# Optimization experiments

Measured on AMD Instinct MI355X. Metric: run time of the kernel, lower is better.

Reference implementation:

```python
import jax, jax.numpy as jnp
import numpy as np

DIM = 192
HEADS = 4


def setup_inputs() -> dict:
    key = jax.random.key(0)
    ks = jax.random.split(key, 6)
    b, h, w = 8, 128, 128
    return {
        "x": jax.random.normal(ks[0], (b, DIM, h, w), jnp.float32),
        "svp_fea": jax.random.normal(ks[1], (b, 3, h, w), jnp.float32),
        "qkv_w": jax.random.normal(ks[2], (3 * DIM, DIM), jnp.float32) * 0.02,
        "dw_w": jax.random.normal(ks[3], (3 * DIM, 1, 3, 3), jnp.float32) * 0.02,
        "svp_w": jax.random.normal(ks[4], (3 * HEADS, 3), jnp.float32) * 0.02,
        "proj_w": jax.random.normal(ks[5], (DIM, DIM + 3 * HEADS), jnp.float32) * 0.02,
        "temperature": jnp.ones((HEADS, 1, 1), jnp.float32),
    }


def _l2norm(t):
    # F.normalize(t, dim=-1): divide by max(||t||_2, eps)
    return t / jnp.maximum(jnp.linalg.norm(t, axis=-1, keepdims=True), 1e-12)


def reference(x, svp_fea, qkv_w, dw_w, svp_w, proj_w, temperature):
    b, c, h, w = x.shape
    heads = temperature.shape[0]
    # 1x1 conv (dim -> 3*dim), then 3x3 depthwise conv (groups = 3*dim)
    qkv = jnp.einsum('bchw,oc->bohw', x, qkv_w)
    qkv = jax.lax.conv_general_dilated(
        qkv, dw_w, window_strides=(1, 1), padding=((1, 1), (1, 1)),
        dimension_numbers=('NCHW', 'OIHW', 'NCHW'), feature_group_count=3 * c)
    # 1x1 conv on illumination prior: 3 -> 3*heads
    svp_q = jnp.einsum('bchw,oc->bohw', svp_fea, svp_w)
    q, k, v = jnp.split(qkv, 3, axis=1)
    ch = c // heads
    hw = h * w
    q = _l2norm(q.reshape(b, heads, ch, hw))
    k = _l2norm(k.reshape(b, heads, ch, hw))
    v = v.reshape(b, heads, ch, hw)
    sq = _l2norm(svp_q.reshape(b, heads, 3, hw))
    q = jnp.concatenate([q, sq], axis=2)            # [b, head, ch+3, hw]
    logits = jnp.einsum('bhcn,bhdn->bhcd', q, k) * temperature[None]
    attn = jax.nn.softmax(logits, axis=-1)          # softmax over channel dim d
    out = jnp.einsum('bhcd,bhdn->bhcn', attn, v)    # [b, head, ch+3, hw]
    out = out.reshape(b, heads * (ch + 3), h, w)
    return jnp.einsum('bchw,oc->bohw', out, proj_w)
```

## Files before the change

kernel.cpp:

```cpp
#include <hip/hip_runtime.h>
#include <hip/hip_bf16.h>
#include <math.h>

#define BB   8
#define CCH  192
#define OCN  576
#define HWD  128
#define HWN  16384
#define NH   4
#define CHD  48
#define C51  51
#define GSZ  (C51*48)

typedef __hip_bfloat16 bf16;
typedef __attribute__((ext_vector_type(8))) short short8;
typedef __attribute__((ext_vector_type(4))) float f32x4;

__device__ __forceinline__ float bfbits2f(unsigned int u16) {
  union { unsigned int i; float f; } v; v.i = u16 << 16; return v.f;
}
__device__ __forceinline__ unsigned short f2bfbits(float f) {
  __hip_bfloat16 h = __float2bfloat16(f);
  return *(unsigned short*)&h;
}
__device__ __forceinline__ void stage16(const void* g, void* l) {
  __builtin_amdgcn_global_load_lds(
      (const __attribute__((address_space(1))) void*)g,
      (__attribute__((address_space(3))) void*)l, 16, 0, 0);
}

__global__ __launch_bounds__(256) void k_svp(
    const float* __restrict__ svp_fea, const float* __restrict__ svp_w,
    float* __restrict__ svp_q, float* __restrict__ ssq_svp_p)
{
  __shared__ float lsw[4][12];
  const int b = blockIdx.y;
  const int t = threadIdx.x;
  const int n = blockIdx.x * 256 + t;
  const int wave = t >> 6;
  const float* fb = svp_fea + (size_t)b * 3 * HWN;
  const float f0 = fb[n], f1 = fb[HWN + n], f2 = fb[2 * HWN + n];
  float* ob = svp_q + (size_t)b * 12 * HWN + n;
  #pragma unroll
  for (int r = 0; r < 12; ++r) {
    float o = svp_w[r*3]*f0 + svp_w[r*3+1]*f1 + svp_w[r*3+2]*f2;
    ob[(size_t)r * HWN] = o;
    float v = o * o;
    #pragma unroll
    for (int off = 32; off >= 1; off >>= 1) v += __shfl_down(v, off, 64);
    if ((t & 63) == 0) lsw[wave][r] = v;
  }
  __syncthreads();
  if (t < 12) {
    float s = lsw[0][t] + lsw[1][t] + lsw[2][t] + lsw[3][t];
    ssq_svp_p[((size_t)b * 12 + t) * 64 + blockIdx.x] = s;
  }
}

__global__ __launch_bounds__(256) void k_castw(
    const float* __restrict__ w, unsigned short* __restrict__ wb)
{
  const int i = (blockIdx.x * 256 + threadIdx.x) * 4;
  float4 v = *(const float4*)(w + i);
  union { uint2 u; unsigned short s[4]; } pk;
  pk.s[0] = f2bfbits(v.x); pk.s[1] = f2bfbits(v.y);
  pk.s[2] = f2bfbits(v.z); pk.s[3] = f2bfbits(v.w);
  *(uint2*)(wb + i) = pk.u;
}

__global__ __launch_bounds__(256) void k_gemm(
    const float* __restrict__ x, const unsigned short* __restrict__ wb,
    unsigned short* __restrict__ qkv1)
{
  __shared__ unsigned short Xs[64 * CCH];
  __shared__ unsigned short Wd[2][32 * CCH];
  const int b = blockIdx.y;
  const int n0 = blockIdx.x * 64;
  const int t = threadIdx.x;
  const int lane = t & 63, wave = t >> 6;
  const int wm = wave >> 1, wn = wave & 1;
  const int lq = lane >> 4, lr = lane & 15;

  #pragma unroll
  for (int i = 0; i < 3; ++i) {
    int chunk = wave * 3 + i;
    int d = chunk * 64 + lane;
    int row = d / 24, kg = d % 24;
    int skg = (kg & ~7) | ((kg & 7) ^ (row & 7));
    stage16(wb + (size_t)row * CCH + skg * 8, &Wd[0][0] + chunk * 512);
  }

  const float* xb = x + (size_t)b * CCH * HWN + n0;
  #pragma unroll
  for (int rr = 0; rr < 6; ++rr) {
    int idx = rr * 256 + t;
    int cp = idx >> 4, nq = idx & 15;
    int c0 = cp * 2;
    float4 v0 = *(const float4*)(xb + (size_t)c0 * HWN + nq * 4);
    float4 v1 = *(const float4*)(xb + (size_t)(c0 + 1) * HWN + nq * 4);
    int g = c0 >> 3, co = c0 & 7;
    float a0[4] = {v0.x, v0.y, v0.z, v0.w};
    float a1[4] = {v1.x, v1.y, v1.z, v1.w};
    #pragma unroll
    for (int j = 0; j < 4; ++j) {
      int n = nq * 4 + j;
      int gs = (g & ~7) | ((g & 7) ^ (n & 7) ^ ((n >> 3) & 7));
      unsigned int pk = (unsigned int)f2bfbits(a0[j])
                      | ((unsigned int)f2bfbits(a1[j]) << 16);
      *(unsigned int*)&Xs[n * CCH + gs * 8 + co] = pk;
    }
  }
  __syncthreads();

  short8 bfr[2][6];
  #pragma unroll
  for (int nf = 0; nf < 2; ++nf) {
    int r = wn * 32 + nf * 16 + lr;
    #pragma unroll
    for (int ks = 0; ks < 6; ++ks) {
      int gk = ks * 4 + lq;
      int sg = (gk & ~7) | ((gk & 7) ^ (r & 7) ^ ((r >> 3) & 7));
      bfr[nf][ks] = *(const short8*)&Xs[r * CCH + sg * 8];
    }
  }

  for (int mc = 0; mc < 18; ++mc) {
    if (mc + 1 < 18) {
      const unsigned short* wsrc = wb + (size_t)(mc + 1) * 32 * CCH;
      unsigned short* nb = &Wd[(mc + 1) & 1][0];
      #pragma unroll
      for (int i = 0; i < 3; ++i) {
        int chunk = wave * 3 + i;
        int d = chunk * 64 + lane;
        int row = d / 24, kg = d % 24;
        int skg = (kg & ~7) | ((kg & 7) ^ (row & 7));
        stage16(wsrc + (size_t)row * CCH + skg * 8, nb + chunk * 512);
      }
      asm volatile("s_waitcnt vmcnt(3)" ::: "memory");
    } else {
      asm volatile("s_waitcnt vmcnt(0)" ::: "memory");
    }
    __builtin_amdgcn_s_barrier();
    asm volatile("" ::: "memory");

    const unsigned short* wbuf = &Wd[mc & 1][0];
    f32x4 acc0 = (f32x4)0.f, acc1 = (f32x4)0.f;
    #pragma unroll
    for (int ks = 0; ks < 6; ++ks) {
      const int gk = ks * 4 + lq;
      int r = wm * 16 + lr;
      int sg = (gk & ~7) | ((gk & 7) ^ (r & 7));
      short8 a = *(const short8*)&wbuf[r * CCH + sg * 8];
      acc0 = __builtin_amdgcn_mfma_f32_16x16x32_bf16(a, bfr[0][ks], acc0, 0, 0, 0);
      acc1 = __builtin_amdgcn_mfma_f32_16x16x32_bf16(a, bfr[1][ks], acc1, 0, 0, 0);
    }

    unsigned short* ob = qkv1 + ((size_t)b * OCN + mc * 32 + wm * 16) * HWN
                         + n0 + wn * 32;
    #pragma unroll
    for (int r = 0; r < 4; ++r) {
      ob[(size_t)(lq * 4 + r) * HWN + lr]      = f2bfbits(acc0[r]);
      ob[(size_t)(lq * 4 + r) * HWN + 16 + lr] = f2bfbits(acc1[r]);
    }
    asm volatile("" ::: "memory");
    __builtin_amdgcn_s_barrier();
  }
}

__global__ __launch_bounds__(256) void k_dw(
    const unsigned short* __restrict__ qkv1, const float* __restrict__ dw_w,
    unsigned short* __restrict__ qkv, float* __restrict__ ssq_qk_p)
{
  __shared__ float lsw[4];
  const int b = blockIdx.z, c = blockIdx.y, slab = blockIdx.x;
  const int t = threadIdx.x;
  const int cg = t & 15, rg = t >> 4;
  const int y0 = slab * 32 + rg * 2;
  const unsigned short* src = qkv1 + ((size_t)b * OCN + c) * HWN;
  float w[9];
  #pragma unroll
  for (int i = 0; i < 9; ++i) w[i] = dw_w[c * 9 + i];

  float rows[4][10];
  #pragma unroll
  for (int j = 0; j < 4; ++j) {
    int gr = y0 - 1 + j;
    uint4 B = make_uint4(0u, 0u, 0u, 0u);
    unsigned int Al = 0; unsigned int Cv = 0;
    if ((unsigned)gr < 128u) {
      const unsigned short* rp = src + (size_t)gr * HWD;
      B = *(const uint4*)(rp + cg * 8);
      if (cg > 0)  Al = *(const unsigned int*)(rp + cg * 8 - 2);
      if (cg < 15) Cv = (unsigned int)rp[cg * 8 + 8];
    }
    rows[j][0] = bfbits2f(Al >> 16);
    unsigned int ub[4] = {B.x, B.y, B.z, B.w};
    #pragma unroll
    for (int q = 0; q < 4; ++q) {
      rows[j][1 + 2*q] = bfbits2f(ub[q] & 0xffffu);
      rows[j][2 + 2*q] = bfbits2f(ub[q] >> 16);
    }
    rows[j][9] = bfbits2f(Cv);
  }

  unsigned short* dst = qkv + ((size_t)b * OCN + c) * HWN;
  float ssq = 0.f;
  #pragma unroll
  for (int e = 0; e < 2; ++e) {
    float acc[8];
    #pragma unroll
    for (int i = 0; i < 8; ++i) acc[i] = 0.f;
    #pragma unroll
    for (int j = 0; j < 3; ++j) {
      const float* vr = rows[e + j];
      #pragma unroll
      for (int i = 0; i < 8; ++i)
        acc[i] += w[j*3]*vr[i] + w[j*3+1]*vr[i+1] + w[j*3+2]*vr[i+2];
    }
    union { uint4 u; unsigned short s[8]; } pk;
    #pragma unroll
    for (int i = 0; i < 8; ++i) pk.s[i] = f2bfbits(acc[i]);
    *(uint4*)(dst + (size_t)(y0 + e) * HWD + cg * 8) = pk.u;
    if (c < 384) {
      #pragma unroll
      for (int i = 0; i < 8; ++i) {
        float rv = bfbits2f(pk.s[i]);
        ssq += rv * rv;
      }
    }
  }
  if (c < 384) {
    #pragma unroll
    for (int off = 32; off >= 1; off >>= 1) ssq += __shfl_down(ssq, off, 64);
    if ((t & 63) == 0) lsw[t >> 6] = ssq;
  }
  __syncthreads();
  if (c < 384 && t == 0)
    ssq_qk_p[(((size_t)b * 384 + c) << 2) | slab] =
        lsw[0] + lsw[1] + lsw[2] + lsw[3];
}

__global__ __launch_bounds__(256) void k_gram(
    const unsigned short* __restrict__ qkv, const float* __restrict__ svp_q,
    float* __restrict__ Gp)
{
  __shared__ float Gs[C51 * 50];
  const int chunk = blockIdx.x, h = blockIdx.y, b = blockIdx.z;
  const int t = threadIdx.x;
  const int lane = t & 63, wave = t >> 6;
  const int lq = lane >> 4, lr = lane & 15;
  const unsigned short* qb = qkv + ((size_t)b*OCN + h*CHD)*HWN;
  const unsigned short* kb = qkv + ((size_t)b*OCN + 192 + h*CHD)*HWN;
  const float* sb = svp_q + ((size_t)b*12 + h*3)*HWN;

  for (int idx = t; idx < C51*50; idx += 256) Gs[idx] = 0.f;

  f32x4 acc[3][3], sacc[3];
  #pragma unroll
  for (int mf = 0; mf < 3; ++mf)
    #pragma unroll
    for (int nf = 0; nf < 3; ++nf) acc[mf][nf] = (f32x4)0.f;
  #pragma unroll
  for (int nf = 0; nf < 3; ++nf) sacc[nf] = (f32x4)0.f;

  const int nbase = chunk * 1024 + wave * 256;
  #pragma unroll 4
  for (int ks = 0; ks < 8; ++ks) {
    const int n = nbase + ks * 32 + lq * 8;
    short8 a[3], bb[3];
    #pragma unroll
    for (int mf = 0; mf < 3; ++mf)
      a[mf] = *(const short8*)&qb[(size_t)(mf*16 + lr)*HWN + n];
    #pragma unroll
    for (int nf = 0; nf < 3; ++nf)
      bb[nf] = *(const short8*)&kb[(size_t)(nf*16 + lr)*HWN + n];
    union { short8 s8; unsigned short us[8]; } sv;
    #pragma unroll
    for (int i = 0; i < 8; ++i) sv.us[i] = 0;
    if (lr < 3) {
      const float* sp = sb + (size_t)lr*HWN + n;
      float4 v0 = *(const float4*)sp, v1 = *(const float4*)(sp + 4);
      sv.us[0] = f2bfbits(v0.x); sv.us[1] = f2bfbits(v0.y);
      sv.us[2] = f2bfbits(v0.z); sv.us[3] = f2bfbits(v0.w);
      sv.us[4] = f2bfbits(v1.x); sv.us[5] = f2bfbits(v1.y);
      sv.us[6] = f2bfbits(v1.z); sv.us[7] = f2bfbits(v1.w);
    }
    #pragma unroll
    for (int mf = 0; mf < 3; ++mf)
      #pragma unroll
      for (int nf = 0; nf < 3; ++nf)
        acc[mf][nf] = __builtin_amdgcn_mfma_f32_16x16x32_bf16(
            a[mf], bb[nf], acc[mf][nf], 0, 0, 0);
    #pragma unroll
    for (int nf = 0; nf < 3; ++nf)
      sacc[nf] = __builtin_amdgcn_mfma_f32_16x16x32_bf16(
          sv.s8, bb[nf], sacc[nf], 0, 0, 0);
  }

  __syncthreads();
  for (int w = 0; w < 4; ++w) {
    if (wave == w) {
      #pragma unroll
      for (int mf = 0; mf < 3; ++mf)
        #pragma unroll
        for (int nf = 0; nf < 3; ++nf)
          #pragma unroll
          for (int r = 0; r < 4; ++r)
            Gs[(mf*16 + lq*4 + r)*50 + nf*16 + lr] += acc[mf][nf][r];
      if (lq == 0) {
        #pragma unroll
        for (int nf = 0; nf < 3; ++nf)
          #pragma unroll
          for (int r = 0; r < 3; ++r)
            Gs[(48 + r)*50 + nf*16 + lr] += sacc[nf][r];
      }
    }
    __syncthreads();
  }
  float* Gout = Gp + ((size_t)((b*NH + h) * 16 + chunk)) * GSZ;
  for (int idx = t; idx < GSZ; idx += 256) {
    int row = idx / 48, col = idx - row * 48;
    Gout[idx] = Gs[row*50 + col];
  }
}

__global__ __launch_bounds__(256) void k_attn_fold(
    const float* __restrict__ Gp, const float* __restrict__ ssq_qk_p,
    const float* __restrict__ ssq_svp_p, const float* __restrict__ temperature,
    const float* __restrict__ proj_w, unsigned short* __restrict__ W2bf)
{
  __shared__ float A[GSZ];
  __shared__ float qinv[C51];
  __shared__ float kinv[48];
  const int h = blockIdx.x, b = blockIdx.y;
  const int t = threadIdx.x;
  const float* Gb = Gp + ((size_t)(b*NH + h) * 16) * GSZ;
  if (t < 48) {
    const float* p = ssq_qk_p + (((size_t)b * 384 + 192 + h*48 + t) << 2);
    kinv[t] = 1.f / fmaxf(sqrtf(p[0] + p[1] + p[2] + p[3]), 1e-12f);
  }
  if (t >= 64 && t < 64 + C51) {
    int c = t - 64;
    float ss;
    if (c < 48) {
      const float* p = ssq_qk_p + (((size_t)b * 384 + h*48 + c) << 2);
      ss = p[0] + p[1] + p[2] + p[3];
    } else {
      const float* p = ssq_svp_p + ((size_t)b * 12 + h*3 + (c - 48)) * 64;
      float s0 = 0.f, s1 = 0.f, s2 = 0.f, s3 = 0.f;
      #pragma unroll
      for (int i = 0; i < 16; ++i) {
        float4 v = *(const float4*)(p + i * 4);
        s0 += v.x; s1 += v.y; s2 += v.z; s3 += v.w;
      }
      ss = (s0 + s1) + (s2 + s3);
    }
    qinv[c] = 1.f / fmaxf(sqrtf(ss), 1e-12f);
  }
  for (int idx = t; idx < GSZ; idx += 256) {
    float s = 0.f;
    #pragma unroll
    for (int c = 0; c < 16; ++c) s += Gb[(size_t)c * GSZ + idx];
    A[idx] = s;
  }
  __syncthreads();
  const float temp = temperature[h];
  if (t < C51) {
    float row[48];
    float m = -1e30f;
    const float qi = qinv[t] * temp;
    #pragma unroll
    for (int d = 0; d < 48; ++d) {
      float l = A[t*48 + d] * qi * kinv[d];
      row[d] = l; m = fmaxf(m, l);
    }
    float s = 0.f;
    #pragma unroll
    for (int d = 0; d < 48; ++d) { row[d] = expf(row[d] - m); s += row[d]; }
    const float inv = 1.f / s;
    #pragma unroll
    for (int d = 0; d < 48; ++d) A[t*48 + d] = row[d] * inv;
  }
  __syncthreads();
  for (int idx = t; idx < 192*48; idx += 256) {
    int o = idx / 48, d = idx - o*48;
    const float* pw = proj_w + o*204 + C51*h;
    float s = 0.f;
    #pragma unroll
    for (int c = 0; c < C51; ++c) s += pw[c] * A[c*48 + d];
    W2bf[((size_t)b*CCH + o)*CCH + h*48 + d] = f2bfbits(s);
  }
}

__global__ __launch_bounds__(256) void k_out(
    const unsigned short* __restrict__ qkv, const unsigned short* __restrict__ w2b,
    float* __restrict__ out)
{
  __shared__ unsigned short Vs[64 * CCH];
  __shared__ unsigned short Wd[2][32 * CCH];
  const int b = blockIdx.y;
  const int n0 = blockIdx.x * 64;
  const int t = threadIdx.x;
  const int lane = t & 63, wave = t >> 6;
  const int wm = wave >> 1, wn = wave & 1;
  const int lq = lane >> 4, lr = lane & 15;

  const unsigned short* w2base = w2b + (size_t)b * CCH * CCH;
  #pragma unroll
  for (int i = 0; i < 3; ++i) {
    int chunk = wave * 3 + i;
    int d = chunk * 64 + lane;
    int row = d / 24, kg = d % 24;
    int skg = (kg & ~7) | ((kg & 7) ^ (row & 7));
    stage16(w2base + (size_t)row * CCH + skg * 8, &Wd[0][0] + chunk * 512);
  }

  const unsigned short* vb = qkv + ((size_t)b * OCN + 384) * HWN + n0;
  #pragma unroll
  for (int rr = 0; rr < 3; ++rr) {
    int idx = rr * 256 + t;
    int cp = idx >> 3, nq = idx & 7;
    int c0 = cp * 2;
    uint4 v0 = *(const uint4*)(vb + (size_t)c0 * HWN + nq * 8);
    uint4 v1 = *(const uint4*)(vb + (size_t)(c0 + 1) * HWN + nq * 8);
    union { uint4 u; unsigned short s[8]; } p0, p1;
    p0.u = v0; p1.u = v1;
    int g = c0 >> 3, co = c0 & 7;
    #pragma unroll
    for (int j = 0; j < 8; ++j) {
      int n = nq * 8 + j;
      int gs = (g & ~7) | ((g & 7) ^ (n & 7) ^ ((n >> 3) & 7));
      unsigned int pk = (unsigned int)p0.s[j] | ((unsigned int)p1.s[j] << 16);
      *(unsigned int*)&Vs[n * CCH + gs * 8 + co] = pk;
    }
  }
  __syncthreads();

  short8 bfr[2][6];
  #pragma unroll
  for (int nf = 0; nf < 2; ++nf) {
    int r = wn * 32 + nf * 16 + lr;
    #pragma unroll
    for (int ks = 0; ks < 6; ++ks) {
      int gk = ks * 4 + lq;
      int sg = (gk & ~7) | ((gk & 7) ^ (r & 7) ^ ((r >> 3) & 7));
      bfr[nf][ks] = *(const short8*)&Vs[r * CCH + sg * 8];
    }
  }

  for (int mc = 0; mc < 6; ++mc) {
    if (mc + 1 < 6) {
      const unsigned short* wsrc = w2base + (size_t)(mc + 1) * 32 * CCH;
      unsigned short* nb = &Wd[(mc + 1) & 1][0];
      #pragma unroll
      for (int i = 0; i < 3; ++i) {
        int chunk = wave * 3 + i;
        int d = chunk * 64 + lane;
        int row = d / 24, kg = d % 24;
        int skg = (kg & ~7) | ((kg & 7) ^ (row & 7));
        stage16(wsrc + (size_t)row * CCH + skg * 8, nb + chunk * 512);
      }
      asm volatile("s_waitcnt vmcnt(3)" ::: "memory");
    } else {
      asm volatile("s_waitcnt vmcnt(0)" ::: "memory");
    }
    __builtin_amdgcn_s_barrier();
    asm volatile("" ::: "memory");

    const unsigned short* wbuf = &Wd[mc & 1][0];
    f32x4 acc0 = (f32x4)0.f, acc1 = (f32x4)0.f;
    #pragma unroll
    for (int ks = 0; ks < 6; ++ks) {
      const int gk = ks * 4 + lq;
      int r = wm * 16 + lr;
      int sg = (gk & ~7) | ((gk & 7) ^ (r & 7));
      short8 a = *(const short8*)&wbuf[r * CCH + sg * 8];
      acc0 = __builtin_amdgcn_mfma_f32_16x16x32_bf16(a, bfr[0][ks], acc0, 0, 0, 0);
      acc1 = __builtin_amdgcn_mfma_f32_16x16x32_bf16(a, bfr[1][ks], acc1, 0, 0, 0);
    }

    float* ob = out + ((size_t)b * CCH + mc * 32 + wm * 16) * HWN + n0 + wn * 32;
    #pragma unroll
    for (int r = 0; r < 4; ++r) {
      ob[(size_t)(lq * 4 + r) * HWN + lr]      = acc0[r];
      ob[(size_t)(lq * 4 + r) * HWN + 16 + lr] = acc1[r];
    }
    asm volatile("" ::: "memory");
    __builtin_amdgcn_s_barrier();
  }
}

extern "C" void kernel_launch(void* const* d_in, const int* in_sizes, int n_in,
                              void* d_out, int out_size, void* d_ws, size_t ws_size,
                              hipStream_t stream)
{
  const float* x       = (const float*)d_in[0];
  const float* svp_fea = (const float*)d_in[1];
  const float* qkv_w   = (const float*)d_in[2];
  const float* dw_w    = (const float*)d_in[3];
  const float* svp_w   = (const float*)d_in[4];
  const float* proj_w  = (const float*)d_in[5];
  const float* temp    = (const float*)d_in[6];
  float* outp = (float*)d_out;

  char* ws = (char*)d_ws;
  const size_t off_qkv1   = 0;
  const size_t off_qkv    = off_qkv1  + (size_t)BB*OCN*HWN*2;
  const size_t off_wb     = off_qkv   + (size_t)BB*OCN*HWN*2;
  const size_t off_svpq   = off_wb    + (size_t)OCN*CCH*2;
  const size_t off_ssqqk  = off_svpq  + (size_t)BB*12*HWN*4;
  const size_t off_ssqsvp = off_ssqqk + (size_t)BB*384*4*4;
  const size_t off_Gp     = off_ssqsvp+ (size_t)BB*12*64*4;
  const size_t off_W2     = off_Gp    + (size_t)BB*NH*16*GSZ*4;

  unsigned short* qkv1  = (unsigned short*)(ws + off_qkv1);
  bf16*  qkv     = (bf16*)(ws + off_qkv);
  unsigned short* wb    = (unsigned short*)(ws + off_wb);
  float* svp_q   = (float*)(ws + off_svpq);
  float* ssq_qk_p  = (float*)(ws + off_ssqqk);
  float* ssq_svp_p = (float*)(ws + off_ssqsvp);
  float* Gp      = (float*)(ws + off_Gp);
  unsigned short* W2bf  = (unsigned short*)(ws + off_W2);

  k_castw    <<<dim3(108),         256, 0, stream>>>(qkv_w, wb);
  k_svp      <<<dim3(64, BB),      256, 0, stream>>>(svp_fea, svp_w, svp_q, ssq_svp_p);
  k_gemm     <<<dim3(256, BB),     256, 0, stream>>>(x, wb, qkv1);
  k_dw       <<<dim3(4, OCN, BB),  256, 0, stream>>>(qkv1, dw_w, (unsigned short*)qkv, ssq_qk_p);
  k_gram     <<<dim3(16, NH, BB),  256, 0, stream>>>((const unsigned short*)qkv, svp_q, Gp);
  k_attn_fold<<<dim3(NH, BB),      256, 0, stream>>>(Gp, ssq_qk_p, ssq_svp_p, temp, proj_w, W2bf);
  k_out      <<<dim3(256, BB),     256, 0, stream>>>((const unsigned short*)qkv, W2bf, outp);
}
```

Baseline: 279.5 us.

## Widen QKV GEMM pixel tile and swap MFMA operands for vectorized stores

```diff
diff --git a/kernel.cpp b/kernel.cpp
--- a/kernel.cpp
+++ b/kernel.cpp
@@ -72,10 +72,10 @@
     const float* __restrict__ x, const unsigned short* __restrict__ wb,
     unsigned short* __restrict__ qkv1)
 {
-  __shared__ unsigned short Xs[64 * CCH];
+  __shared__ unsigned short Xs[128 * CCH];
   __shared__ unsigned short Wd[2][32 * CCH];
   const int b = blockIdx.y;
-  const int n0 = blockIdx.x * 64;
+  const int n0 = blockIdx.x * 128;
   const int t = threadIdx.x;
   const int lane = t & 63, wave = t >> 6;
   const int wm = wave >> 1, wn = wave & 1;
@@ -92,9 +92,9 @@
 
   const float* xb = x + (size_t)b * CCH * HWN + n0;
   #pragma unroll
-  for (int rr = 0; rr < 6; ++rr) {
+  for (int rr = 0; rr < 12; ++rr) {
     int idx = rr * 256 + t;
-    int cp = idx >> 4, nq = idx & 15;
+    int cp = idx >> 5, nq = idx & 31;
     int c0 = cp * 2;
     float4 v0 = *(const float4*)(xb + (size_t)c0 * HWN + nq * 4);
     float4 v1 = *(const float4*)(xb + (size_t)(c0 + 1) * HWN + nq * 4);
@@ -112,10 +112,10 @@
   }
   __syncthreads();
 
-  short8 bfr[2][6];
-  #pragma unroll
-  for (int nf = 0; nf < 2; ++nf) {
-    int r = wn * 32 + nf * 16 + lr;
+  short8 bfr[4][6];
+  #pragma unroll
+  for (int nf = 0; nf < 4; ++nf) {
+    int r = wn * 64 + nf * 16 + lr;
     #pragma unroll
     for (int ks = 0; ks < 6; ++ks) {
       int gk = ks * 4 + lq;
@@ -144,23 +144,30 @@
     asm volatile("" ::: "memory");
 
     const unsigned short* wbuf = &Wd[mc & 1][0];
-    f32x4 acc0 = (f32x4)0.f, acc1 = (f32x4)0.f;
+    f32x4 acc[4];
+    #pragma unroll
+    for (int nf = 0; nf < 4; ++nf) acc[nf] = (f32x4)0.f;
+
     #pragma unroll
     for (int ks = 0; ks < 6; ++ks) {
       const int gk = ks * 4 + lq;
-      int r = wm * 16 + lr;
-      int sg = (gk & ~7) | ((gk & 7) ^ (r & 7));
-      short8 a = *(const short8*)&wbuf[r * CCH + sg * 8];
-      acc0 = __builtin_amdgcn_mfma_f32_16x16x32_bf16(a, bfr[0][ks], acc0, 0, 0, 0);
-      acc1 = __builtin_amdgcn_mfma_f32_16x16x32_bf16(a, bfr[1][ks], acc1, 0, 0, 0);
-    }
-
-    unsigned short* ob = qkv1 + ((size_t)b * OCN + mc * 32 + wm * 16) * HWN
-                         + n0 + wn * 32;
-    #pragma unroll
-    for (int r = 0; r < 4; ++r) {
-      ob[(size_t)(lq * 4 + r) * HWN + lr]      = f2bfbits(acc0[r]);
-      ob[(size_t)(lq * 4 + r) * HWN + 16 + lr] = f2bfbits(acc1[r]);
+      int rW = wm * 16 + lr;
+      int sg = (gk & ~7) | ((gk & 7) ^ (rW & 7));
+      short8 w8 = *(const short8*)&wbuf[rW * CCH + sg * 8];
+      #pragma unroll
+      for (int nf = 0; nf < 4; ++nf)
+        acc[nf] = __builtin_amdgcn_mfma_f32_16x16x32_bf16(
+            bfr[nf][ks], w8, acc[nf], 0, 0, 0);
+    }
+
+    unsigned short* ob = qkv1 + ((size_t)b * OCN + mc * 32 + wm * 16 + lr) * HWN
+                         + n0 + wn * 64 + lq * 4;
+    #pragma unroll
+    for (int nf = 0; nf < 4; ++nf) {
+      union { uint2 u; unsigned short s[4]; } pk;
+      #pragma unroll
+      for (int r = 0; r < 4; ++r) pk.s[r] = f2bfbits(acc[nf][r]);
+      *(uint2*)(ob + nf * 16) = pk.u;
     }
     asm volatile("" ::: "memory");
     __builtin_amdgcn_s_barrier();
@@ -472,19 +479,17 @@
     #pragma unroll
     for (int ks = 0; ks < 6; ++ks) {
       const int gk = ks * 4 + lq;
-      int r = wm * 16 + lr;
-      int sg = (gk & ~7) | ((gk & 7) ^ (r & 7));
-      short8 a = *(const short8*)&wbuf[r * CCH + sg * 8];
-      acc0 = __builtin_amdgcn_mfma_f32_16x16x32_bf16(a, bfr[0][ks], acc0, 0, 0, 0);
-      acc1 = __builtin_amdgcn_mfma_f32_16x16x32_bf16(a, bfr[1][ks], acc1, 0, 0, 0);
-    }
-
-    float* ob = out + ((size_t)b * CCH + mc * 32 + wm * 16) * HWN + n0 + wn * 32;
-    #pragma unroll
-    for (int r = 0; r < 4; ++r) {
-      ob[(size_t)(lq * 4 + r) * HWN + lr]      = acc0[r];
-      ob[(size_t)(lq * 4 + r) * HWN + 16 + lr] = acc1[r];
-    }
+      int rW = wm * 16 + lr;
+      int sg = (gk & ~7) | ((gk & 7) ^ (rW & 7));
+      short8 w8 = *(const short8*)&wbuf[rW * CCH + sg * 8];
+      acc0 = __builtin_amdgcn_mfma_f32_16x16x32_bf16(bfr[0][ks], w8, acc0, 0, 0, 0);
+      acc1 = __builtin_amdgcn_mfma_f32_16x16x32_bf16(bfr[1][ks], w8, acc1, 0, 0, 0);
+    }
+
+    float* ob = out + ((size_t)b * CCH + mc * 32 + wm * 16 + lr) * HWN
+                + n0 + wn * 32 + lq * 4;
+    *(f32x4*)ob = acc0;
+    *(f32x4*)(ob + 16) = acc1;
     asm volatile("" ::: "memory");
     __builtin_amdgcn_s_barrier();
   }
@@ -524,7 +529,7 @@
 
   k_castw    <<<dim3(108),         256, 0, stream>>>(qkv_w, wb);
   k_svp      <<<dim3(64, BB),      256, 0, stream>>>(svp_fea, svp_w, svp_q, ssq_svp_p);
-  k_gemm     <<<dim3(256, BB),     256, 0, stream>>>(x, wb, qkv1);
+  k_gemm     <<<dim3(128, BB),     256, 0, stream>>>(x, wb, qkv1);
   k_dw       <<<dim3(4, OCN, BB),  256, 0, stream>>>(qkv1, dw_w, (unsigned short*)qkv, ssq_qk_p);
   k_gram     <<<dim3(16, NH, BB),  256, 0, stream>>>((const unsigned short*)qkv, svp_q, Gp);
   k_attn_fold<<<dim3(NH, BB),      256, 0, stream>>>(Gp, ssq_qk_p, ssq_svp_p, temp, proj_w, W2bf);
```

Measured after the change: 279.3 us. No clear change (-0.1%).
